# Performance work log

Measured on AMD Instinct MI355X. Metric: run time of the kernel, lower is better.

The kernel has to match this reference:

```python
import jax, jax.numpy as jnp
import numpy as np

B, S, W = 1024, 256, 16      # batch, max_sentence_size, max chars per word bag
NB_CLASSES = 256             # character vocabulary
EMB = 50                     # embedding_size (hardcoded in source)


def setup_inputs() -> dict:
    key = jax.random.key(0)
    k1, k2, k3 = jax.random.split(key, 3)
    # per-word bags of character indices (padded to W); original code applies
    # np.unique per bag, so we treat entries as already deduplicated indices.
    chars = jax.random.randint(k1, (B, S, W), 0, NB_CLASSES, dtype=jnp.int32)
    # number of valid chars per bag, in [1, W] (original bags are non-empty)
    lengths = jax.random.randint(k2, (B, S), 1, W + 1, dtype=jnp.int32)
    emb_table = jax.random.normal(k3, (NB_CLASSES, EMB), dtype=jnp.float32)
    return {"chars": chars, "lengths": lengths, "emb_table": emb_table}


def reference(chars, lengths, emb_table):
    # EmbeddingBag(mode='mean') over ragged bags, vectorized:
    # gather: [B, S, W, EMB]
    gathered = emb_table[chars]
    # mask padded slots within each bag
    mask = (jnp.arange(W)[None, None, :] < lengths[:, :, None]).astype(emb_table.dtype)
    summed = jnp.einsum('bswe,bsw->bse', gathered, mask)
    out = summed / lengths[:, :, None].astype(emb_table.dtype)  # [B, S, EMB]
    return out
```

## Files before the change

### kernel.cpp

```cpp
#include <hip/hip_runtime.h>


constexpr int EMB     = 50;
constexpr int RSTRIDE = 56;
constexpr int TBL_F   = 256 * RSTRIDE;
constexpr int NBAGS   = 1024 * 256;
constexpr int BLOCK   = 1024;
constexpr int TPB     = 13;
constexpr int BPP     = BLOCK / TPB;
constexpr int CHUNK   = 512;
constexpr int NPASS   = (CHUNK + BPP - 1) / BPP;
constexpr int BLOCKS  = NBAGS / CHUNK;

__global__ __launch_bounds__(BLOCK, 8) void embag_sorted_kernel(
    const int*   __restrict__ chars,
    const int*   __restrict__ lengths,
    const float* __restrict__ table,
    float*       __restrict__ out)
{
    __shared__ float    tbl[TBL_F];
    __shared__ unsigned short order[CHUNK];
    __shared__ unsigned bins[17];
    __shared__ float    invl[17];

    for (int i = threadIdx.x; i < TBL_F; i += BLOCK) {
        const int r = i / RSTRIDE;
        const int c = i - r * RSTRIDE;
        tbl[i] = (c < EMB) ? table[r * EMB + c] : 0.0f;
    }
    if (threadIdx.x < 17) {
        bins[threadIdx.x] = 0;
        invl[threadIdx.x] = threadIdx.x ? 1.0f / (float)threadIdx.x : 0.0f;
    }
    __syncthreads();

    const int base = blockIdx.x * CHUNK;

    int myLen = 0, myTicket = 0;
    if (threadIdx.x < CHUNK) {
        myLen = lengths[base + threadIdx.x];
        myTicket = atomicAdd(&bins[myLen], 1u);
    }
    __syncthreads();
    if (threadIdx.x == 0) {
        unsigned s = 0;
        for (int l = 1; l <= 16; ++l) { unsigned c = bins[l]; bins[l] = s; s += c; }
    }
    __syncthreads();
    if (threadIdx.x < CHUNK)
        order[bins[myLen] + myTicket] =
            (unsigned short)((myLen << 9) | threadIdx.x);
    __syncthreads();

    const int  lb     = threadIdx.x / TPB;
    const int  t      = threadIdx.x - lb * TPB;
    const bool active = (lb < BPP);
    const float* rowp = tbl + 4 * t;

    for (int p = 0; p < NPASS; ++p) {
        const int oi = p * BPP + lb;
        if (!active || oi >= CHUNK) continue;

        const unsigned o   = order[oi];
        const int      len = (int)(o >> 9);
        const int      bag = base + (int)(o & 511u);

        const int4* cp = reinterpret_cast<const int4*>(chars + (size_t)bag * 16);
        const int4 c0 = cp[0], c1 = cp[1], c2 = cp[2], c3 = cp[3];

        float4 acc = make_float4(0.f, 0.f, 0.f, 0.f);

        #define G(comp)                                                        \
            {                                                                  \
                const float4 v =                                               \
                    *reinterpret_cast<const float4*>(rowp + (comp) * RSTRIDE); \
                acc.x += v.x; acc.y += v.y; acc.z += v.z; acc.w += v.w;        \
            }

        G(c0.x)
        if (len > 1)  { G(c0.y)
        if (len > 2)  { G(c0.z)
        if (len > 3)  { G(c0.w)
        if (len > 4)  { G(c1.x)
        if (len > 5)  { G(c1.y)
        if (len > 6)  { G(c1.z)
        if (len > 7)  { G(c1.w)
        if (len > 8)  { G(c2.x)
        if (len > 9)  { G(c2.y)
        if (len > 10) { G(c2.z)
        if (len > 11) { G(c2.w)
        if (len > 12) { G(c3.x)
        if (len > 13) { G(c3.y)
        if (len > 14) { G(c3.z)
        if (len > 15) { G(c3.w) }}}}}}}}}}}}}}}
        #undef G

        const float inv = invl[len];
        float* ob = out + (size_t)bag * EMB + 4u * (unsigned)t;
        reinterpret_cast<float2*>(ob)[0] = make_float2(acc.x * inv, acc.y * inv);
        if (t < 12)
            reinterpret_cast<float2*>(ob)[1] = make_float2(acc.z * inv, acc.w * inv);
    }
}

extern "C" void kernel_launch(void* const* d_in, const int* in_sizes, int n_in,
                              void* d_out, int out_size, void* d_ws, size_t ws_size,
                              hipStream_t stream) {
    const int*   chars   = (const int*)d_in[0];
    const int*   lengths = (const int*)d_in[1];
    const float* table   = (const float*)d_in[2];
    float*       out     = (float*)d_out;

    embag_sorted_kernel<<<dim3(BLOCKS), dim3(BLOCK), 0, stream>>>(
        chars, lengths, table, out);
}
```

Before: 29.71 us.

## Drop per-block length sort and prefetch next bag's char indices

Removes the shared-memory counting sort of bags by length (atomics, serial prefix scan, extra barriers) and instead loads lengths into shared memory with vector loads, processing bags in natural order. Each thread group now software-pipelines the global loads of the next bag's character indices while accumulating the current bag. This cuts setup latency and hides global load latency, but gives up the length-sorted ordering, so lanes in a wavefront may diverge more on ragged bag lengths. It also adds register pressure for the double-buffered index vectors.

Measured after the change: 24.88 us. -16.3%, faster.

```diff
diff --git a/kernel.cpp b/kernel.cpp
--- a/kernel.cpp
+++ b/kernel.cpp
@@ -12,44 +12,28 @@
 constexpr int NPASS   = (CHUNK + BPP - 1) / BPP;
 constexpr int BLOCKS  = NBAGS / CHUNK;
 
-__global__ __launch_bounds__(BLOCK, 8) void embag_sorted_kernel(
+__global__ __launch_bounds__(BLOCK, 8) void embag_pipe_kernel(
     const int*   __restrict__ chars,
     const int*   __restrict__ lengths,
     const float* __restrict__ table,
     float*       __restrict__ out)
 {
-    __shared__ float    tbl[TBL_F];
-    __shared__ unsigned short order[CHUNK];
-    __shared__ unsigned bins[17];
-    __shared__ float    invl[17];
+    __shared__ float tbl[TBL_F];
+    __shared__ int   lenbuf[CHUNK];
+    __shared__ float invl[17];
+
+    const int base = blockIdx.x * CHUNK;
 
     for (int i = threadIdx.x; i < TBL_F; i += BLOCK) {
         const int r = i / RSTRIDE;
         const int c = i - r * RSTRIDE;
         tbl[i] = (c < EMB) ? table[r * EMB + c] : 0.0f;
     }
-    if (threadIdx.x < 17) {
-        bins[threadIdx.x] = 0;
+    if (threadIdx.x < CHUNK / 4)
+        reinterpret_cast<int4*>(lenbuf)[threadIdx.x] =
+            reinterpret_cast<const int4*>(lengths + base)[threadIdx.x];
+    if (threadIdx.x < 17)
         invl[threadIdx.x] = threadIdx.x ? 1.0f / (float)threadIdx.x : 0.0f;
-    }
-    __syncthreads();
-
-    const int base = blockIdx.x * CHUNK;
-
-    int myLen = 0, myTicket = 0;
-    if (threadIdx.x < CHUNK) {
-        myLen = lengths[base + threadIdx.x];
-        myTicket = atomicAdd(&bins[myLen], 1u);
-    }
-    __syncthreads();
-    if (threadIdx.x == 0) {
-        unsigned s = 0;
-        for (int l = 1; l <= 16; ++l) { unsigned c = bins[l]; bins[l] = s; s += c; }
-    }
-    __syncthreads();
-    if (threadIdx.x < CHUNK)
-        order[bins[myLen] + myTicket] =
-            (unsigned short)((myLen << 9) | threadIdx.x);
     __syncthreads();
 
     const int  lb     = threadIdx.x / TPB;
@@ -57,49 +41,54 @@
     const bool active = (lb < BPP);
     const float* rowp = tbl + 4 * t;
 
+    int idx = active ? lb : 0;
+    const int4* cp = reinterpret_cast<const int4*>(chars + (size_t)(base + idx) * 16);
+    int4 c0 = cp[0], c1 = cp[1], c2 = cp[2], c3 = cp[3];
+
     for (int p = 0; p < NPASS; ++p) {
-        const int oi = p * BPP + lb;
-        if (!active || oi >= CHUNK) continue;
+        const int idxn = (idx + BPP < CHUNK) ? idx + BPP : CHUNK - 1;
+        const int4* cpn =
+            reinterpret_cast<const int4*>(chars + (size_t)(base + idxn) * 16);
+        const int4 n0 = cpn[0], n1 = cpn[1], n2 = cpn[2], n3 = cpn[3];
 
-        const unsigned o   = order[oi];
-        const int      len = (int)(o >> 9);
-        const int      bag = base + (int)(o & 511u);
+        if (active && idx < CHUNK) {
+            const int len = lenbuf[idx];
 
-        const int4* cp = reinterpret_cast<const int4*>(chars + (size_t)bag * 16);
-        const int4 c0 = cp[0], c1 = cp[1], c2 = cp[2], c3 = cp[3];
+            float4 acc = make_float4(0.f, 0.f, 0.f, 0.f);
 
-        float4 acc = make_float4(0.f, 0.f, 0.f, 0.f);
+            #define G(comp)                                                        \
+                {                                                                  \
+                    const float4 v =                                               \
+                        *reinterpret_cast<const float4*>(rowp + (comp) * RSTRIDE); \
+                    acc.x += v.x; acc.y += v.y; acc.z += v.z; acc.w += v.w;        \
+                }
+            G(c0.x)
+            if (len > 1)  { G(c0.y)
+            if (len > 2)  { G(c0.z)
+            if (len > 3)  { G(c0.w)
+            if (len > 4)  { G(c1.x)
+            if (len > 5)  { G(c1.y)
+            if (len > 6)  { G(c1.z)
+            if (len > 7)  { G(c1.w)
+            if (len > 8)  { G(c2.x)
+            if (len > 9)  { G(c2.y)
+            if (len > 10) { G(c2.z)
+            if (len > 11) { G(c2.w)
+            if (len > 12) { G(c3.x)
+            if (len > 13) { G(c3.y)
+            if (len > 14) { G(c3.z)
+            if (len > 15) { G(c3.w) }}}}}}}}}}}}}}}
+            #undef G
 
-        #define G(comp)                                                        \
-            {                                                                  \
-                const float4 v =                                               \
-                    *reinterpret_cast<const float4*>(rowp + (comp) * RSTRIDE); \
-                acc.x += v.x; acc.y += v.y; acc.z += v.z; acc.w += v.w;        \
-            }
+            const float inv = invl[len];
+            float* ob = out + (size_t)(base + idx) * EMB + 4u * (unsigned)t;
+            reinterpret_cast<float2*>(ob)[0] = make_float2(acc.x * inv, acc.y * inv);
+            if (t < 12)
+                reinterpret_cast<float2*>(ob)[1] = make_float2(acc.z * inv, acc.w * inv);
+        }
 
-        G(c0.x)
-        if (len > 1)  { G(c0.y)
-        if (len > 2)  { G(c0.z)
-        if (len > 3)  { G(c0.w)
-        if (len > 4)  { G(c1.x)
-        if (len > 5)  { G(c1.y)
-        if (len > 6)  { G(c1.z)
-        if (len > 7)  { G(c1.w)
-        if (len > 8)  { G(c2.x)
-        if (len > 9)  { G(c2.y)
-        if (len > 10) { G(c2.z)
-        if (len > 11) { G(c2.w)
-        if (len > 12) { G(c3.x)
-        if (len > 13) { G(c3.y)
-        if (len > 14) { G(c3.z)
-        if (len > 15) { G(c3.w) }}}}}}}}}}}}}}}
-        #undef G
-
-        const float inv = invl[len];
-        float* ob = out + (size_t)bag * EMB + 4u * (unsigned)t;
-        reinterpret_cast<float2*>(ob)[0] = make_float2(acc.x * inv, acc.y * inv);
-        if (t < 12)
-            reinterpret_cast<float2*>(ob)[1] = make_float2(acc.z * inv, acc.w * inv);
+        c0 = n0; c1 = n1; c2 = n2; c3 = n3;
+        idx += BPP;
     }
 }
 
@@ -111,6 +100,6 @@
     const float* table   = (const float*)d_in[2];
     float*       out     = (float*)d_out;
 
-    embag_sorted_kernel<<<dim3(BLOCKS), dim3(BLOCK), 0, stream>>>(
+    embag_pipe_kernel<<<dim3(BLOCKS), dim3(BLOCK), 0, stream>>>(
         chars, lengths, table, out);
 }
```
